# Optimization experiments

Hardware: AMD Instinct MI355X
Metric: run time of the kernel (lower is better)

## Reference

```python
import jax, jax.numpy as jnp
import numpy as np

M, K, N = 65536, 512, 512
EPS = 1e-05


def setup_inputs() -> dict:
    key = jax.random.key(0)
    k1, k2, k3 = jax.random.split(key, 3)
    x = jax.random.normal(k1, (M, K), dtype=jnp.float32)
    # int8 weight buffer in [-128, 127]
    weight_int8 = jax.random.randint(k2, (N, K), -128, 128, dtype=jnp.int32).astype(jnp.int8)
    # realistic per-output-channel dequant scales (max-abs / 127 of an fp weight)
    weight_scale = jax.random.uniform(k3, (N,), dtype=jnp.float32, minval=0.001, maxval=0.02)
    return {"x": x, "weight_int8": weight_int8, "weight_scale": weight_scale}


def reference(x, weight_int8, weight_scale):
    # dynamic per-tensor quantization of the activation
    x_scale = jnp.maximum(jnp.max(jnp.abs(x)) / 127.0, EPS)
    x_int8 = jnp.clip(jnp.round(x / x_scale), -128, 127).astype(jnp.int8)
    out_int32 = jnp.matmul(x_int8, weight_int8.T, preferred_element_type=jnp.int32)
    # dequantize: per-tensor input scale * per-row weight scale
    out = out_int32.astype(jnp.float32) * (x_scale * weight_scale[None, :])
    return out
```

## Files before the change

kernel.cpp:

```cpp
#include <hip/hip_runtime.h>


#define M_DIM 65536
#define K_DIM 512
#define N_DIM 512
#define EPSF  1e-5f

typedef int int32x4 __attribute__((ext_vector_type(4)));

#define WS_PART   256
#define WS_WPACK  32768
#define WS_X8     294912
#define WS_NEEDED ((size_t)WS_X8 + (size_t)M_DIM * K_DIM)

__device__ inline unsigned int pack_w4(int4 v) {
    return (v.x & 0xff) | ((v.y & 0xff) << 8) |
           ((v.z & 0xff) << 16) | ((unsigned)v.w << 24);
}

__device__ inline unsigned int quantpack4(float4 f, float inv) {
    const float C = 12582912.0f;
    unsigned int u0 = __float_as_uint(fmaf(f.x, inv, C));
    unsigned int u1 = __float_as_uint(fmaf(f.y, inv, C));
    unsigned int u2 = __float_as_uint(fmaf(f.z, inv, C));
    unsigned int u3 = __float_as_uint(fmaf(f.w, inv, C));
    unsigned int lo = __builtin_amdgcn_perm(u1, u0, 0x0C0C0400u);
    unsigned int hi = __builtin_amdgcn_perm(u3, u2, 0x04000C0Cu);
    return lo | hi;
}

__global__ void absmax1_pack_kernel(const float* __restrict__ x,
                                    const int* __restrict__ wi,
                                    float* __restrict__ partials,
                                    unsigned int* __restrict__ wp) {
    const int b = blockIdx.x;
    const int t = threadIdx.x;
    if (b < 4096) {
        __shared__ float red[4];
        const float4* x4 = (const float4*)x;
        const int base = b * 2048;
        float m = 0.0f;
        #pragma unroll
        for (int j = 0; j < 8; ++j) {
            float4 v = x4[base + j * 256 + t];
            m = fmaxf(m, fmaxf(fmaxf(fabsf(v.x), fabsf(v.y)),
                               fmaxf(fabsf(v.z), fabsf(v.w))));
        }
        #pragma unroll
        for (int off = 32; off > 0; off >>= 1)
            m = fmaxf(m, __shfl_xor(m, off));
        if ((t & 63) == 0) red[t >> 6] = m;
        __syncthreads();
        if (t == 0)
            partials[b] = fmaxf(fmaxf(red[0], red[1]), fmaxf(red[2], red[3]));
    } else {
        const int bb = b - 4096;
        #pragma unroll
        for (int j = 0; j < 4; ++j) {
            int d = bb * 1024 + j * 256 + t;
            wp[d] = pack_w4(((const int4*)wi)[d]);
        }
    }
}

__global__ void quant_kernel(const float* __restrict__ x,
                             const float* __restrict__ partials,
                             unsigned int* __restrict__ ws_abs,
                             unsigned int* __restrict__ x8) {
    __shared__ float red[4];
    const int t = threadIdx.x;
    const float4* p4 = (const float4*)partials;
    float m = 0.0f;
    #pragma unroll
    for (int j = 0; j < 4; ++j) {
        float4 v = p4[t + j * 256];
        m = fmaxf(m, fmaxf(fmaxf(v.x, v.y), fmaxf(v.z, v.w)));
    }
    #pragma unroll
    for (int off = 32; off > 0; off >>= 1)
        m = fmaxf(m, __shfl_xor(m, off));
    if ((t & 63) == 0) red[t >> 6] = m;
    __syncthreads();
    m = fmaxf(fmaxf(red[0], red[1]), fmaxf(red[2], red[3]));
    const float s   = fmaxf(m / 127.0f, EPSF);
    const float inv = 1.0f / s;
    if (blockIdx.x == 0 && t == 0) ws_abs[0] = __float_as_uint(s);

    const float4* x4 = (const float4*)x;
    const int base = blockIdx.x * 4096;
    #pragma unroll
    for (int j = 0; j < 16; ++j) {
        int idx = base + j * 256 + t;
        x8[idx] = quantpack4(x4[idx], inv);
    }
}

__global__ void absmax2_kernel(const float* __restrict__ partials,
                               unsigned int* __restrict__ ws) {
    __shared__ float red[4];
    const int t = threadIdx.x;
    const float4* p4 = (const float4*)partials;
    float m = 0.0f;
    #pragma unroll
    for (int j = 0; j < 4; ++j) {
        float4 v = p4[t + j * 256];
        m = fmaxf(m, fmaxf(fmaxf(v.x, v.y), fmaxf(v.z, v.w)));
    }
    #pragma unroll
    for (int off = 32; off > 0; off >>= 1)
        m = fmaxf(m, __shfl_xor(m, off));
    if ((t & 63) == 0) red[t >> 6] = m;
    __syncthreads();
    if (t == 0)
        ws[0] = __float_as_uint(fmaxf(fmaxf(red[0], red[1]),
                                      fmaxf(red[2], red[3])));
}

__global__ __launch_bounds__(256, 2) void gemm8_kernel(
    const signed char* __restrict__ x8, const signed char* __restrict__ w,
    const float* __restrict__ wscale, const unsigned int* __restrict__ ws,
    float* __restrict__ out) {
    __shared__ signed char Blds[64 * 1024];

    const int wave = threadIdx.x >> 6;
    const int lane = threadIdx.x & 63;
    const int quad = lane >> 4;
    const int l16  = lane & 15;

    const int id  = blockIdx.x;
    const int xcd = id & 7;
    const int j   = id >> 3;
    const int by  = xcd * 64 + (j >> 2);
    const int bx  = j & 3;
    const int m0 = by * 128;
    const int n0 = bx * 128;

    #pragma unroll
    for (int cc = 0; cc < 2; ++cc) {
        int c = wave * 2 + cc;
        #pragma unroll
        for (int t = 0; t < 8; ++t) {
            const signed char* g = w + (long)(n0 + t * 16 + l16) * K_DIM
                                     + c * 64 + quad * 16;
            __builtin_amdgcn_global_load_lds(
                (const __attribute__((address_space(1))) unsigned int*)g,
                (__attribute__((address_space(3))) unsigned int*)(Blds + (c * 8 + t) * 1024),
                16, 0, 0);
        }
    }

    const float s = __uint_as_float(ws[0]);

    const int mw = m0 + wave * 32;
    const signed char* xr0 = x8 + (long)(mw + l16) * K_DIM + quad * 16;
    const signed char* xr1 = xr0 + (long)16 * K_DIM;

    int32x4 acc0[8] = {};
    int32x4 acc1[8] = {};

    __syncthreads();

    #pragma unroll
    for (int k0 = 0; k0 < K_DIM; k0 += 64) {
        int32x4 a0 = *(const int32x4*)(xr0 + k0);
        int32x4 a1 = *(const int32x4*)(xr1 + k0);
        const signed char* bbase = Blds + (k0 >> 6) * 8192 + lane * 16;
        #pragma unroll
        for (int t = 0; t < 8; ++t) {
            int32x4 b = *(const int32x4*)(bbase + t * 1024);
            acc0[t] = __builtin_amdgcn_mfma_i32_16x16x64_i8(a0, b, acc0[t], 0, 0, 0);
            acc1[t] = __builtin_amdgcn_mfma_i32_16x16x64_i8(a1, b, acc1[t], 0, 0, 0);
        }
    }

    #pragma unroll
    for (int t = 0; t < 8; ++t) {
        int n = n0 + t * 16 + l16;
        float c = s * wscale[n];
        float* o0 = out + (long)(mw + quad * 4) * N_DIM + n;
        float* o1 = o0 + (long)16 * N_DIM;
        #pragma unroll
        for (int r = 0; r < 4; ++r) {
            o0[(long)r * N_DIM] = (float)acc0[t][r] * c;
            o1[(long)r * N_DIM] = (float)acc1[t][r] * c;
        }
    }
}

__global__ __launch_bounds__(256, 2) void gemm_f32_kernel(
    const float* __restrict__ x, const signed char* __restrict__ w,
    const float* __restrict__ wscale, const unsigned int* __restrict__ ws,
    float* __restrict__ out) {
    __shared__ signed char Blds[64 * 1024];

    const int wave = threadIdx.x >> 6;
    const int lane = threadIdx.x & 63;
    const int quad = lane >> 4;
    const int l16  = lane & 15;

    const int id  = blockIdx.x;
    const int xcd = id & 7;
    const int j   = id >> 3;
    const int by  = xcd * 64 + (j >> 2);
    const int bx  = j & 3;
    const int m0 = by * 128;
    const int n0 = bx * 128;

    #pragma unroll
    for (int cc = 0; cc < 2; ++cc) {
        int c = wave * 2 + cc;
        #pragma unroll
        for (int t = 0; t < 8; ++t) {
            const signed char* g = w + (long)(n0 + t * 16 + l16) * K_DIM
                                     + c * 64 + quad * 16;
            __builtin_amdgcn_global_load_lds(
                (const __attribute__((address_space(1))) unsigned int*)g,
                (__attribute__((address_space(3))) unsigned int*)(Blds + (c * 8 + t) * 1024),
                16, 0, 0);
        }
    }

    float mx  = __uint_as_float(ws[0]);
    float s   = fmaxf(mx / 127.0f, EPSF);
    float inv = 1.0f / s;

    const int mw = m0 + wave * 32;
    const float* xr0 = x + (long)(mw + l16) * K_DIM + quad * 16;
    const float* xr1 = xr0 + (long)16 * K_DIM;

    int32x4 acc0[8] = {};
    int32x4 acc1[8] = {};

    __syncthreads();

    #pragma unroll
    for (int k0 = 0; k0 < K_DIM; k0 += 64) {
        const float4* xp0 = (const float4*)(xr0 + k0);
        const float4* xp1 = (const float4*)(xr1 + k0);
        float4 f0 = xp0[0], f1 = xp0[1], f2 = xp0[2], f3 = xp0[3];
        float4 g0 = xp1[0], g1 = xp1[1], g2 = xp1[2], g3 = xp1[3];
        int32x4 a0, a1;
        a0.x = (int)quantpack4(f0, inv);
        a0.y = (int)quantpack4(f1, inv);
        a0.z = (int)quantpack4(f2, inv);
        a0.w = (int)quantpack4(f3, inv);
        a1.x = (int)quantpack4(g0, inv);
        a1.y = (int)quantpack4(g1, inv);
        a1.z = (int)quantpack4(g2, inv);
        a1.w = (int)quantpack4(g3, inv);

        const signed char* bbase = Blds + (k0 >> 6) * 8192 + lane * 16;
        #pragma unroll
        for (int t = 0; t < 8; ++t) {
            int32x4 b = *(const int32x4*)(bbase + t * 1024);
            acc0[t] = __builtin_amdgcn_mfma_i32_16x16x64_i8(a0, b, acc0[t], 0, 0, 0);
            acc1[t] = __builtin_amdgcn_mfma_i32_16x16x64_i8(a1, b, acc1[t], 0, 0, 0);
        }
    }

    #pragma unroll
    for (int t = 0; t < 8; ++t) {
        int n = n0 + t * 16 + l16;
        float c = s * wscale[n];
        float* o0 = out + (long)(mw + quad * 4) * N_DIM + n;
        float* o1 = o0 + (long)16 * N_DIM;
        #pragma unroll
        for (int r = 0; r < 4; ++r) {
            o0[(long)r * N_DIM] = (float)acc0[t][r] * c;
            o1[(long)r * N_DIM] = (float)acc1[t][r] * c;
        }
    }
}

extern "C" void kernel_launch(void* const* d_in, const int* in_sizes, int n_in,
                              void* d_out, int out_size, void* d_ws, size_t ws_size,
                              hipStream_t stream) {
    const float* x   = (const float*)d_in[0];
    const int*   wi  = (const int*)d_in[1];
    const float* sc  = (const float*)d_in[2];
    float*       out = (float*)d_out;

    unsigned int* ws_abs   = (unsigned int*)d_ws;
    float*        partials = (float*)((char*)d_ws + WS_PART);
    unsigned int* wp       = (unsigned int*)((char*)d_ws + WS_WPACK);
    unsigned int* x8       = (unsigned int*)((char*)d_ws + WS_X8);
    const signed char* w8  = (const signed char*)wp;

    absmax1_pack_kernel<<<4160, 256, 0, stream>>>(x, wi, partials, wp);

    if (ws_size >= WS_NEEDED) {
        quant_kernel<<<2048, 256, 0, stream>>>(x, partials, ws_abs, x8);
        gemm8_kernel<<<2048, 256, 0, stream>>>((const signed char*)x8, w8, sc,
                                               ws_abs, out);
    } else {
        absmax2_kernel<<<1, 256, 0, stream>>>(partials, ws_abs);
        gemm_f32_kernel<<<2048, 256, 0, stream>>>(x, w8, sc, ws_abs, out);
    }
}
```

Before: 282.5 us.

## Fuse activation quantization into GEMM with per-block row tiles held in registers

Replaces the separate quant kernel and int8 GEMM with one fused kernel. Each block loads 128 rows of fp32 activations, quantizes them into swizzled LDS, moves the int8 A fragments into registers, then loops over the four N tiles, reloading weight tiles into the same LDS. This removes the int8 activation round trip through global memory and one launch. In exchange the grid shrinks to 512 blocks, weight loads are serialized per N tile with no overlap, and register pressure rises.

```diff
diff --git a/kernel.cpp b/kernel.cpp
--- a/kernel.cpp
+++ b/kernel.cpp
@@ -10,8 +10,6 @@
 
 #define WS_PART   256
 #define WS_WPACK  32768
-#define WS_X8     294912
-#define WS_NEEDED ((size_t)WS_X8 + (size_t)M_DIM * K_DIM)
 
 __device__ inline unsigned int pack_w4(int4 v) {
     return (v.x & 0xff) | ((v.y & 0xff) << 8) |
@@ -63,212 +61,121 @@
     }
 }
 
-__global__ void quant_kernel(const float* __restrict__ x,
-                             const float* __restrict__ partials,
-                             unsigned int* __restrict__ ws_abs,
-                             unsigned int* __restrict__ x8) {
+__global__ __launch_bounds__(256, 2) void fused_quant_gemm_kernel(
+    const float* __restrict__ x, const signed char* __restrict__ w,
+    const float* __restrict__ wscale, const float* __restrict__ partials,
+    float* __restrict__ out) {
+    __shared__ __attribute__((aligned(16))) signed char Lds[64 * 1024];
     __shared__ float red[4];
-    const int t = threadIdx.x;
-    const float4* p4 = (const float4*)partials;
-    float m = 0.0f;
-    #pragma unroll
-    for (int j = 0; j < 4; ++j) {
-        float4 v = p4[t + j * 256];
-        m = fmaxf(m, fmaxf(fmaxf(v.x, v.y), fmaxf(v.z, v.w)));
-    }
-    #pragma unroll
-    for (int off = 32; off > 0; off >>= 1)
-        m = fmaxf(m, __shfl_xor(m, off));
-    if ((t & 63) == 0) red[t >> 6] = m;
-    __syncthreads();
-    m = fmaxf(fmaxf(red[0], red[1]), fmaxf(red[2], red[3]));
-    const float s   = fmaxf(m / 127.0f, EPSF);
-    const float inv = 1.0f / s;
-    if (blockIdx.x == 0 && t == 0) ws_abs[0] = __float_as_uint(s);
 
-    const float4* x4 = (const float4*)x;
-    const int base = blockIdx.x * 4096;
-    #pragma unroll
-    for (int j = 0; j < 16; ++j) {
-        int idx = base + j * 256 + t;
-        x8[idx] = quantpack4(x4[idx], inv);
-    }
-}
-
-__global__ void absmax2_kernel(const float* __restrict__ partials,
-                               unsigned int* __restrict__ ws) {
-    __shared__ float red[4];
-    const int t = threadIdx.x;
-    const float4* p4 = (const float4*)partials;
-    float m = 0.0f;
-    #pragma unroll
-    for (int j = 0; j < 4; ++j) {
-        float4 v = p4[t + j * 256];
-        m = fmaxf(m, fmaxf(fmaxf(v.x, v.y), fmaxf(v.z, v.w)));
-    }
-    #pragma unroll
-    for (int off = 32; off > 0; off >>= 1)
-        m = fmaxf(m, __shfl_xor(m, off));
-    if ((t & 63) == 0) red[t >> 6] = m;
-    __syncthreads();
-    if (t == 0)
-        ws[0] = __float_as_uint(fmaxf(fmaxf(red[0], red[1]),
-                                      fmaxf(red[2], red[3])));
-}
-
-__global__ __launch_bounds__(256, 2) void gemm8_kernel(
-    const signed char* __restrict__ x8, const signed char* __restrict__ w,
-    const float* __restrict__ wscale, const unsigned int* __restrict__ ws,
-    float* __restrict__ out) {
-    __shared__ signed char Blds[64 * 1024];
-
-    const int wave = threadIdx.x >> 6;
-    const int lane = threadIdx.x & 63;
+    const int t    = threadIdx.x;
+    const int wave = t >> 6;
+    const int lane = t & 63;
     const int quad = lane >> 4;
     const int l16  = lane & 15;
+    const int m0   = blockIdx.x * 128;
 
-    const int id  = blockIdx.x;
-    const int xcd = id & 7;
-    const int j   = id >> 3;
-    const int by  = xcd * 64 + (j >> 2);
-    const int bx  = j & 3;
-    const int m0 = by * 128;
-    const int n0 = bx * 128;
+    float m = 0.0f;
+    {
+        const float4* p4 = (const float4*)partials;
+        #pragma unroll
+        for (int j = 0; j < 4; ++j) {
+            float4 v = p4[t + j * 256];
+            m = fmaxf(m, fmaxf(fmaxf(v.x, v.y), fmaxf(v.z, v.w)));
+        }
+        #pragma unroll
+        for (int off = 32; off > 0; off >>= 1)
+            m = fmaxf(m, __shfl_xor(m, off));
+        if (lane == 0) red[wave] = m;
+    }
+    __syncthreads();
+    const float mx  = fmaxf(fmaxf(red[0], red[1]), fmaxf(red[2], red[3]));
+    const float s   = fmaxf(mx / 127.0f, EPSF);
+    const float inv = 1.0f / s;
+    __syncthreads();
 
-    #pragma unroll
-    for (int cc = 0; cc < 2; ++cc) {
-        int c = wave * 2 + cc;
+    {
+        const float4* xs = (const float4*)(x + (size_t)m0 * K_DIM);
+        const int rsub = t >> 5;
+        const int csub = (t & 31) * 16;
         #pragma unroll
-        for (int t = 0; t < 8; ++t) {
-            const signed char* g = w + (long)(n0 + t * 16 + l16) * K_DIM
-                                     + c * 64 + quad * 16;
-            __builtin_amdgcn_global_load_lds(
-                (const __attribute__((address_space(1))) unsigned int*)g,
-                (__attribute__((address_space(3))) unsigned int*)(Blds + (c * 8 + t) * 1024),
-                16, 0, 0);
+        for (int j = 0; j < 16; ++j) {
+            const int fi = j * 1024 + t * 4;
+            float4 v0 = xs[fi + 0];
+            float4 v1 = xs[fi + 1];
+            float4 v2 = xs[fi + 2];
+            float4 v3 = xs[fi + 3];
+            int32x4 p;
+            p.x = (int)quantpack4(v0, inv);
+            p.y = (int)quantpack4(v1, inv);
+            p.z = (int)quantpack4(v2, inv);
+            p.w = (int)quantpack4(v3, inv);
+            const int row  = j * 8 + rsub;
+            const int addr = (row * 512 + csub) ^ ((row & 7) << 4);
+            *(int32x4*)(Lds + addr) = p;
         }
     }
+    __syncthreads();
 
-    const float s = __uint_as_float(ws[0]);
+    int32x4 a0[8], a1[8];
+    {
+        const int r0 = wave * 32 + l16;
+        const int r1 = r0 + 16;
+        #pragma unroll
+        for (int k = 0; k < 8; ++k) {
+            const int c = quad * 16 + k * 64;
+            a0[k] = *(const int32x4*)(Lds + ((r0 * 512 + c) ^ ((r0 & 7) << 4)));
+            a1[k] = *(const int32x4*)(Lds + ((r1 * 512 + c) ^ ((r1 & 7) << 4)));
+        }
+    }
+    __syncthreads();
 
     const int mw = m0 + wave * 32;
-    const signed char* xr0 = x8 + (long)(mw + l16) * K_DIM + quad * 16;
-    const signed char* xr1 = xr0 + (long)16 * K_DIM;
 
-    int32x4 acc0[8] = {};
-    int32x4 acc1[8] = {};
+    for (int bx = 0; bx < 4; ++bx) {
+        const int n0 = bx * 128;
 
-    __syncthreads();
+        #pragma unroll
+        for (int cc = 0; cc < 2; ++cc) {
+            int c = wave * 2 + cc;
+            #pragma unroll
+            for (int tt = 0; tt < 8; ++tt) {
+                const signed char* g = w + (long)(n0 + tt * 16 + l16) * K_DIM
+                                         + c * 64 + quad * 16;
+                __builtin_amdgcn_global_load_lds(
+                    (const __attribute__((address_space(1))) unsigned int*)g,
+                    (__attribute__((address_space(3))) unsigned int*)(Lds + (c * 8 + tt) * 1024),
+                    16, 0, 0);
+            }
+        }
+        __syncthreads();
 
-    #pragma unroll
-    for (int k0 = 0; k0 < K_DIM; k0 += 64) {
-        int32x4 a0 = *(const int32x4*)(xr0 + k0);
-        int32x4 a1 = *(const int32x4*)(xr1 + k0);
-        const signed char* bbase = Blds + (k0 >> 6) * 8192 + lane * 16;
+        int32x4 acc0[8] = {};
+        int32x4 acc1[8] = {};
         #pragma unroll
-        for (int t = 0; t < 8; ++t) {
-            int32x4 b = *(const int32x4*)(bbase + t * 1024);
-            acc0[t] = __builtin_amdgcn_mfma_i32_16x16x64_i8(a0, b, acc0[t], 0, 0, 0);
-            acc1[t] = __builtin_amdgcn_mfma_i32_16x16x64_i8(a1, b, acc1[t], 0, 0, 0);
+        for (int k = 0; k < 8; ++k) {
+            const signed char* bbase = Lds + k * 8192 + lane * 16;
+            #pragma unroll
+            for (int tt = 0; tt < 8; ++tt) {
+                int32x4 b = *(const int32x4*)(bbase + tt * 1024);
+                acc0[tt] = __builtin_amdgcn_mfma_i32_16x16x64_i8(a0[k], b, acc0[tt], 0, 0, 0);
+                acc1[tt] = __builtin_amdgcn_mfma_i32_16x16x64_i8(a1[k], b, acc1[tt], 0, 0, 0);
+            }
         }
-    }
 
-    #pragma unroll
-    for (int t = 0; t < 8; ++t) {
-        int n = n0 + t * 16 + l16;
-        float c = s * wscale[n];
-        float* o0 = out + (long)(mw + quad * 4) * N_DIM + n;
-        float* o1 = o0 + (long)16 * N_DIM;
         #pragma unroll
-        for (int r = 0; r < 4; ++r) {
-            o0[(long)r * N_DIM] = (float)acc0[t][r] * c;
-            o1[(long)r * N_DIM] = (float)acc1[t][r] * c;
+        for (int tt = 0; tt < 8; ++tt) {
+            int n = n0 + tt * 16 + l16;
+            float c = s * wscale[n];
+            float* o0 = out + (long)(mw + quad * 4) * N_DIM + n;
+            float* o1 = o0 + (long)16 * N_DIM;
+            #pragma unroll
+            for (int r = 0; r < 4; ++r) {
+                o0[(long)r * N_DIM] = (float)acc0[tt][r] * c;
+                o1[(long)r * N_DIM] = (float)acc1[tt][r] * c;
+            }
         }
-    }
-}
-
-__global__ __launch_bounds__(256, 2) void gemm_f32_kernel(
-    const float* __restrict__ x, const signed char* __restrict__ w,
-    const float* __restrict__ wscale, const unsigned int* __restrict__ ws,
-    float* __restrict__ out) {
-    __shared__ signed char Blds[64 * 1024];
-
-    const int wave = threadIdx.x >> 6;
-    const int lane = threadIdx.x & 63;
-    const int quad = lane >> 4;
-    const int l16  = lane & 15;
-
-    const int id  = blockIdx.x;
-    const int xcd = id & 7;
-    const int j   = id >> 3;
-    const int by  = xcd * 64 + (j >> 2);
-    const int bx  = j & 3;
-    const int m0 = by * 128;
-    const int n0 = bx * 128;
-
-    #pragma unroll
-    for (int cc = 0; cc < 2; ++cc) {
-        int c = wave * 2 + cc;
-        #pragma unroll
-        for (int t = 0; t < 8; ++t) {
-            const signed char* g = w + (long)(n0 + t * 16 + l16) * K_DIM
-                                     + c * 64 + quad * 16;
-            __builtin_amdgcn_global_load_lds(
-                (const __attribute__((address_space(1))) unsigned int*)g,
-                (__attribute__((address_space(3))) unsigned int*)(Blds + (c * 8 + t) * 1024),
-                16, 0, 0);
-        }
-    }
-
-    float mx  = __uint_as_float(ws[0]);
-    float s   = fmaxf(mx / 127.0f, EPSF);
-    float inv = 1.0f / s;
-
-    const int mw = m0 + wave * 32;
-    const float* xr0 = x + (long)(mw + l16) * K_DIM + quad * 16;
-    const float* xr1 = xr0 + (long)16 * K_DIM;
-
-    int32x4 acc0[8] = {};
-    int32x4 acc1[8] = {};
-
-    __syncthreads();
-
-    #pragma unroll
-    for (int k0 = 0; k0 < K_DIM; k0 += 64) {
-        const float4* xp0 = (const float4*)(xr0 + k0);
-        const float4* xp1 = (const float4*)(xr1 + k0);
-        float4 f0 = xp0[0], f1 = xp0[1], f2 = xp0[2], f3 = xp0[3];
-        float4 g0 = xp1[0], g1 = xp1[1], g2 = xp1[2], g3 = xp1[3];
-        int32x4 a0, a1;
-        a0.x = (int)quantpack4(f0, inv);
-        a0.y = (int)quantpack4(f1, inv);
-        a0.z = (int)quantpack4(f2, inv);
-        a0.w = (int)quantpack4(f3, inv);
-        a1.x = (int)quantpack4(g0, inv);
-        a1.y = (int)quantpack4(g1, inv);
-        a1.z = (int)quantpack4(g2, inv);
-        a1.w = (int)quantpack4(g3, inv);
-
-        const signed char* bbase = Blds + (k0 >> 6) * 8192 + lane * 16;
-        #pragma unroll
-        for (int t = 0; t < 8; ++t) {
-            int32x4 b = *(const int32x4*)(bbase + t * 1024);
-            acc0[t] = __builtin_amdgcn_mfma_i32_16x16x64_i8(a0, b, acc0[t], 0, 0, 0);
-            acc1[t] = __builtin_amdgcn_mfma_i32_16x16x64_i8(a1, b, acc1[t], 0, 0, 0);
-        }
-    }
-
-    #pragma unroll
-    for (int t = 0; t < 8; ++t) {
-        int n = n0 + t * 16 + l16;
-        float c = s * wscale[n];
-        float* o0 = out + (long)(mw + quad * 4) * N_DIM + n;
-        float* o1 = o0 + (long)16 * N_DIM;
-        #pragma unroll
-        for (int r = 0; r < 4; ++r) {
-            o0[(long)r * N_DIM] = (float)acc0[t][r] * c;
-            o1[(long)r * N_DIM] = (float)acc1[t][r] * c;
-        }
+        if (bx < 3) __syncthreads();
     }
 }
 
@@ -280,20 +187,10 @@
     const float* sc  = (const float*)d_in[2];
     float*       out = (float*)d_out;
 
-    unsigned int* ws_abs   = (unsigned int*)d_ws;
     float*        partials = (float*)((char*)d_ws + WS_PART);
     unsigned int* wp       = (unsigned int*)((char*)d_ws + WS_WPACK);
-    unsigned int* x8       = (unsigned int*)((char*)d_ws + WS_X8);
     const signed char* w8  = (const signed char*)wp;
 
     absmax1_pack_kernel<<<4160, 256, 0, stream>>>(x, wi, partials, wp);
-
-    if (ws_size >= WS_NEEDED) {
-        quant_kernel<<<2048, 256, 0, stream>>>(x, partials, ws_abs, x8);
-        gemm8_kernel<<<2048, 256, 0, stream>>>((const signed char*)x8, w8, sc,
-                                               ws_abs, out);
-    } else {
-        absmax2_kernel<<<1, 256, 0, stream>>>(partials, ws_abs);
-        gemm_f32_kernel<<<2048, 256, 0, stream>>>(x, w8, sc, ws_abs, out);
-    }
+    fused_quant_gemm_kernel<<<512, 256, 0, stream>>>(x, w8, sc, partials, out);
 }
```

Result: faster. 265.7 us (-6.0%).
